# Optimization experiments

Hardware: AMD Instinct MI355X
Metric: run time of the kernel (lower is better)

Reference implementation:

```python
import jax, jax.numpy as jnp
import numpy as np

B, H, W = 32, 32, 32
C_CNN, C_EFF, HID = 512, 1280, 512


def conv1x1(x, w, b):
    # x: [B, Cin, H, W], w: [Cout, Cin], b: [Cout]
    return jnp.einsum('bchw,oc->bohw', x, w) + b[None, :, None, None]


def setup_inputs() -> dict:
    key = jax.random.key(0)
    ks = jax.random.split(key, 12)
    s = 0.02  # small init scale keeps softmax logits well-conditioned
    return {
        'cnn_features': jax.random.normal(ks[0], (B, C_CNN, H, W), jnp.float32),
        'efficient_features': jax.random.normal(ks[1], (B, C_EFF, H, W), jnp.float32),
        'W_cnn': jax.random.normal(ks[2], (HID, C_CNN), jnp.float32) * s,
        'b_cnn': jnp.zeros((HID,), jnp.float32),
        'W_eff': jax.random.normal(ks[3], (HID, C_EFF), jnp.float32) * s,
        'b_eff': jnp.zeros((HID,), jnp.float32),
        'W_q': jax.random.normal(ks[4], (HID, HID), jnp.float32) * s,
        'b_q': jnp.zeros((HID,), jnp.float32),
        'W_k': jax.random.normal(ks[5], (HID, HID), jnp.float32) * s,
        'b_k': jnp.zeros((HID,), jnp.float32),
        'W_v': jax.random.normal(ks[6], (HID, HID), jnp.float32) * s,
        'b_v': jnp.zeros((HID,), jnp.float32),
        'gamma': jnp.asarray([0.1], jnp.float32),
    }


def reference(cnn_features, efficient_features, W_cnn, b_cnn, W_eff, b_eff,
              W_q, b_q, W_k, b_k, W_v, b_v, gamma):
    cnn_proj = conv1x1(cnn_features, W_cnn, b_cnn)          # [B, HID, H, W]
    eff_proj = conv1x1(efficient_features, W_eff, b_eff)    # [B, HID, H, W]
    b, c, h, w = cnn_proj.shape
    n = h * w
    # 1x1 conv QKV projections then flatten spatial dims into tokens
    q = conv1x1(cnn_proj, W_q, b_q).reshape(b, c, n).transpose(0, 2, 1)  # [B, N, C]
    k = conv1x1(eff_proj, W_k, b_k).reshape(b, c, n)                     # [B, C, N]
    v = conv1x1(eff_proj, W_v, b_v).reshape(b, c, n).transpose(0, 2, 1)  # [B, N, C]
    attn = jax.nn.softmax(jnp.einsum('bnc,bcm->bnm', q, k), axis=-1)     # [B, N, N] (unscaled, as in source)
    out = jnp.einsum('bnm,bmc->bnc', attn, v)                            # [B, N, C]
    out = out.transpose(0, 2, 1).reshape(b, c, h, w)
    return gamma[0] * out + cnn_proj
```

## Files before the change

### kernel.cpp

```cpp
#include <hip/hip_runtime.h>
#include <hip/hip_bf16.h>
#include <cstdint>


typedef __hip_bfloat16 bf16;
typedef __bf16 bf16x8 __attribute__((ext_vector_type(8)));
typedef float f32x4 __attribute__((ext_vector_type(4)));

#define NB   32
#define NTOK 1024
#define NHID 512
#define CEFF 1280
#define WSZ  (NHID*NHID)

struct W4 { const float* s[4]; };
__global__ __launch_bounds__(256) void convert_w4_kernel(W4 w, bf16* __restrict__ dst) {
    int i = blockIdx.x * 256 + threadIdx.x;
    int sel = i >> 18, off = i & (WSZ - 1);
    dst[i] = __float2bfloat16(w.s[sel][off]);
}

__global__ __launch_bounds__(256) void transpose_to_bf16_kernel(const float* __restrict__ in,
                                                                bf16* __restrict__ out,
                                                                int C, int N) {
    __shared__ float tile[32][33];
    const int n0 = blockIdx.x * 32, c0 = blockIdx.y * 32, b = blockIdx.z;
    in  += (size_t)b * C * N;
    out += (size_t)b * N * C;
    const int tx = threadIdx.x, ty = threadIdx.y;
    #pragma unroll
    for (int i = ty; i < 32; i += 8)
        tile[i][tx] = in[(size_t)(c0 + i) * N + n0 + tx];
    __syncthreads();
    #pragma unroll
    for (int i = ty; i < 32; i += 8)
        out[(size_t)(n0 + i) * C + c0 + tx] = __float2bfloat16(tile[tx][i]);
}

__global__ __launch_bounds__(256) void bias_fuse_kernel(
    const float* __restrict__ Wq, const float* __restrict__ Wk, const float* __restrict__ Wv,
    const float* __restrict__ bc, const float* __restrict__ be,
    const float* __restrict__ bq, const float* __restrict__ bk, const float* __restrict__ bv,
    float* __restrict__ bqc, float* __restrict__ bkv) {
    const int r = blockIdx.x, t = threadIdx.x;
    const float* Wrow; const float* vin; float badd; float* dst;
    if (r < 512)       { Wrow = Wq + (size_t)r * 512;          vin = bc; badd = bq[r];        dst = bqc + r; }
    else if (r < 1024) { Wrow = Wk + (size_t)(r - 512) * 512;  vin = be; badd = bk[r - 512];  dst = bkv + (r - 512); }
    else               { Wrow = Wv + (size_t)(r - 1024) * 512; vin = be; badd = bv[r - 1024]; dst = bkv + (r - 512); }
    float s = Wrow[t] * vin[t] + Wrow[t + 256] * vin[t + 256];
    #pragma unroll
    for (int off = 32; off >= 1; off >>= 1) s += __shfl_xor(s, off, 64);
    __shared__ float red[4];
    if ((t & 63) == 0) red[t >> 6] = s;
    __syncthreads();
    if (t == 0) dst[0] = red[0] + red[1] + red[2] + red[3] + badd;
}

__global__ __launch_bounds__(256) void gemm_bt_kernel(
    const bf16* __restrict__ A, long long aStride, int lda,
    const bf16* __restrict__ Bt, long long bStride, int ldb,
    int K, int swiz,
    const float* __restrict__ bias,
    float* __restrict__ outF, long long fStride, int ldf,
    const bf16* __restrict__ residH, const float* __restrict__ gammaPtr,
    const float* __restrict__ rsumIn,
    float* __restrict__ rsumOut,
    bf16* __restrict__ outHt, long long htStride, int ldht, int htMax,
    bf16* __restrict__ outHn, long long hnStride, int ldhn, int hnBase, int doExp)
{
    __shared__ __bf16 lA[2][128 * 32];
    __shared__ __bf16 lB[2][128 * 32];
    __shared__ float lrs[128];

    const int tid  = threadIdx.x;
    const int wave = tid >> 6;
    const int lane = tid & 63;

    int bx, by, bz;
    if (swiz) { bx = (int)blockIdx.y & 7; by = (int)blockIdx.y >> 3; bz = (int)blockIdx.z * 8 + (int)blockIdx.x; }
    else      { bx = (int)blockIdx.x;     by = (int)blockIdx.y;      bz = (int)blockIdx.z; }
    const int m0 = by * 128;
    const int n0 = bx * 128;

    const bf16* Ab = A  + (size_t)bz * aStride;
    const bf16* Bb = Bt + (size_t)bz * bStride;

    const int wm = wave >> 1, wn = wave & 1;
    const int lrow = lane & 15, quad = lane >> 4;

    f32x4 acc[4][4];
    #pragma unroll
    for (int i = 0; i < 4; i++)
        #pragma unroll
        for (int j = 0; j < 4; j++)
            acc[i][j] = (f32x4){0.f, 0.f, 0.f, 0.f};

    const int rowl = lane >> 2;
    const int qsw  = (lane & 3) ^ ((lane >> 3) & 3);
    const bf16* gA0 = Ab + (size_t)(m0 +      wave * 16 + rowl) * lda + qsw * 8;
    const bf16* gA1 = Ab + (size_t)(m0 + 64 + wave * 16 + rowl) * lda + qsw * 8;
    const bf16* gB0 = Bb + (size_t)(n0 +      wave * 16 + rowl) * ldb + qsw * 8;
    const bf16* gB1 = Bb + (size_t)(n0 + 64 + wave * 16 + rowl) * ldb + qsw * 8;
    const int dst0 = (wave * 64) * 8;
    const int dst1 = (256 + wave * 64) * 8;

    const int sw = quad ^ ((lrow >> 1) & 3);
    int aoff[4], boff[4];
    #pragma unroll
    for (int mt = 0; mt < 4; mt++) aoff[mt] = ((wm * 4 + mt) * 64 + lrow * 4 + sw) * 8;
    #pragma unroll
    for (int nt = 0; nt < 4; nt++) boff[nt] = ((wn * 4 + nt) * 64 + lrow * 4 + sw) * 8;

    auto stage = [&](int k0, int b) {
        __builtin_amdgcn_global_load_lds((const __attribute__((address_space(1))) void*)(gA0 + k0),
                                         (__attribute__((address_space(3))) void*)(&lA[b][dst0]), 16, 0, 0);
        __builtin_amdgcn_global_load_lds((const __attribute__((address_space(1))) void*)(gA1 + k0),
                                         (__attribute__((address_space(3))) void*)(&lA[b][dst1]), 16, 0, 0);
        __builtin_amdgcn_global_load_lds((const __attribute__((address_space(1))) void*)(gB0 + k0),
                                         (__attribute__((address_space(3))) void*)(&lB[b][dst0]), 16, 0, 0);
        __builtin_amdgcn_global_load_lds((const __attribute__((address_space(1))) void*)(gB1 + k0),
                                         (__attribute__((address_space(3))) void*)(&lB[b][dst1]), 16, 0, 0);
    };

    auto compute = [&](int b) {
        const __bf16* __restrict__ pA = lA[b];
        const __bf16* __restrict__ pB = lB[b];
        bf16x8 af[4], bfr[4];
        #pragma unroll
        for (int mt = 0; mt < 4; mt++) af[mt]  = *(const bf16x8*)&pA[aoff[mt]];
        #pragma unroll
        for (int nt = 0; nt < 4; nt++) bfr[nt] = *(const bf16x8*)&pB[boff[nt]];
        #pragma unroll
        for (int mt = 0; mt < 4; mt++)
            #pragma unroll
            for (int nt = 0; nt < 4; nt++)
                acc[mt][nt] = __builtin_amdgcn_mfma_f32_16x16x32_bf16(af[mt], bfr[nt], acc[mt][nt], 0, 0, 0);
    };

    stage(0, 0);
    int cur = 0;
    for (int k0 = 32; k0 < K; k0 += 32) {
        stage(k0, cur ^ 1);
        asm volatile("s_waitcnt vmcnt(4)" ::: "memory");
        __builtin_amdgcn_s_barrier();
        asm volatile("" ::: "memory");
        compute(cur);
        asm volatile("s_waitcnt lgkmcnt(0)" ::: "memory");
        __builtin_amdgcn_s_barrier();
        cur ^= 1;
    }
    asm volatile("s_waitcnt vmcnt(0)" ::: "memory");
    __builtin_amdgcn_s_barrier();
    asm volatile("" ::: "memory");
    compute(cur);

    const float gscale = gammaPtr ? gammaPtr[0] : 1.0f;
    float rs[4][4];
    if (rsumOut)
        #pragma unroll
        for (int mt = 0; mt < 4; mt++)
            #pragma unroll
            for (int r = 0; r < 4; r++) rs[mt][r] = 0.f;

    #pragma unroll
    for (int mt = 0; mt < 4; mt++) {
        const int mbase = m0 + wm * 64 + mt * 16 + quad * 4;
        float bv[4];
        #pragma unroll
        for (int r = 0; r < 4; r++) bv[r] = bias ? bias[mbase + r] : 0.f;
        #pragma unroll
        for (int nt = 0; nt < 4; nt++) {
            const int n = n0 + wn * 64 + nt * 16 + lrow;
            float v[4];
            #pragma unroll
            for (int r = 0; r < 4; r++) {
                v[r] = acc[mt][nt][r] + bv[r];
                if (doExp) v[r] = __expf(v[r]);
                if (rsumOut) rs[mt][r] += v[r];
            }
            if (outF) {
                float* p = outF + (size_t)bz * fStride;
                const bf16* rp = residH + (size_t)bz * fStride;
                const float rinv = rsumIn ? 1.0f / rsumIn[(size_t)bz * NTOK + n] : 1.0f;
                #pragma unroll
                for (int r = 0; r < 4; r++) {
                    size_t idx = (size_t)(mbase + r) * ldf + n;
                    p[idx] = gscale * v[r] * rinv + __bfloat162float(rp[idx]);
                }
            }
            if (outHt && mbase < htMax) {
                union { bf16 h[4]; unsigned long long u; } pk;
                #pragma unroll
                for (int r = 0; r < 4; r++) pk.h[r] = __float2bfloat16(v[r]);
                *(unsigned long long*)&outHt[(size_t)bz * htStride + (size_t)n * ldht + mbase] = pk.u;
            }
            if (outHn && mbase >= hnBase) {
                bf16* p = outHn + (size_t)bz * hnStride;
                #pragma unroll
                for (int r = 0; r < 4; r++)
                    p[(size_t)(mbase - hnBase + r) * ldhn + n] = __float2bfloat16(v[r]);
            }
        }
    }

    if (rsumOut) {
        #pragma unroll
        for (int mt = 0; mt < 4; mt++)
            #pragma unroll
            for (int r = 0; r < 4; r++) {
                float s = rs[mt][r];
                s += __shfl_xor(s, 1, 64);
                s += __shfl_xor(s, 2, 64);
                s += __shfl_xor(s, 4, 64);
                s += __shfl_xor(s, 8, 64);
                rs[mt][r] = s;
            }
        if (tid < 128) lrs[tid] = 0.f;
        __syncthreads();
        if (lrow == 0) {
            #pragma unroll
            for (int mt = 0; mt < 4; mt++)
                #pragma unroll
                for (int r = 0; r < 4; r++)
                    atomicAdd(&lrs[wm * 64 + mt * 16 + quad * 4 + r], rs[mt][r]);
        }
        __syncthreads();
        if (tid < 128) atomicAdd(&rsumOut[(size_t)bz * NTOK + m0 + tid], lrs[tid]);
    }
}

extern "C" void kernel_launch(void* const* d_in, const int* in_sizes, int n_in,
                              void* d_out, int out_size, void* d_ws, size_t ws_size,
                              hipStream_t stream) {
    const float* x_cnn = (const float*)d_in[0];
    const float* x_eff = (const float*)d_in[1];
    const float* W_cnn = (const float*)d_in[2];
    const float* b_cnn = (const float*)d_in[3];
    const float* W_eff = (const float*)d_in[4];
    const float* b_eff = (const float*)d_in[5];
    const float* W_q   = (const float*)d_in[6];
    const float* b_q   = (const float*)d_in[7];
    const float* W_k   = (const float*)d_in[8];
    const float* b_k   = (const float*)d_in[9];
    const float* W_v   = (const float*)d_in[10];
    const float* b_v   = (const float*)d_in[11];
    const float* gamma = (const float*)d_in[12];
    float* out = (float*)d_out;

    uint8_t* ws = (uint8_t*)d_ws;
    size_t off = 0;
    auto alloc = [&](size_t bytes) -> uint8_t* {
        uint8_t* p = ws + off;
        off = (off + bytes + 255) & ~(size_t)255;
        return p;
    };

    bf16* Wall  = (bf16*)alloc((size_t)4 * WSZ * 2);
    bf16* Wc_h  = Wall;
    bf16* Wq_h  = Wall + WSZ;
    bf16* Wkv_h = Wall + 2 * (size_t)WSZ;
    bf16* Wct   = (bf16*)alloc((size_t)NHID * NHID * 2);
    bf16* Wet   = (bf16*)alloc((size_t)CEFF * NHID * 2);
    bf16* Wstack= (bf16*)alloc((size_t)1024 * NHID * 2);
    bf16* Wkve  = (bf16*)alloc((size_t)1024 * CEFF * 2);
    float* bstack = (float*)alloc(1024 * 4);
    float* bkv  = (float*)alloc(1024 * 4);
    float* rowSum = (float*)alloc((size_t)NB * NTOK * 4);
    bf16* Xc_t  = (bf16*)alloc((size_t)NB * NTOK * NHID * 2);
    bf16* Xe_t  = (bf16*)alloc((size_t)NB * NTOK * CEFF * 2);
    bf16* resid = (bf16*)alloc((size_t)NB * NHID * NTOK * 2);
    bf16* q_t   = (bf16*)alloc((size_t)NB * NTOK * NHID * 2);
    bf16* k_t   = (bf16*)alloc((size_t)NB * NTOK * NHID * 2);
    bf16* v_nt  = (bf16*)alloc((size_t)NB * NHID * NTOK * 2);
    bf16* P     = Xe_t;

    {
        W4 w; w.s[0] = W_cnn; w.s[1] = W_q; w.s[2] = W_k; w.s[3] = W_v;
        convert_w4_kernel<<<4 * WSZ / 256, 256, 0, stream>>>(w, Wall);
    }
    transpose_to_bf16_kernel<<<dim3(NHID / 32, NHID / 32, 1), dim3(32, 8), 0, stream>>>(W_cnn, Wct, NHID, NHID);
    transpose_to_bf16_kernel<<<dim3(CEFF / 32, NHID / 32, 1), dim3(32, 8), 0, stream>>>(W_eff, Wet, NHID, CEFF);

    transpose_to_bf16_kernel<<<dim3(NTOK / 32, NHID / 32, NB), dim3(32, 8), 0, stream>>>(x_cnn, Xc_t, NHID, NTOK);
    transpose_to_bf16_kernel<<<dim3(NTOK / 32, CEFF / 32, NB), dim3(32, 8), 0, stream>>>(x_eff, Xe_t, CEFF, NTOK);

    bias_fuse_kernel<<<1536, 256, 0, stream>>>(W_q, W_k, W_v, b_cnn, b_eff, b_q, b_k, b_v, bstack, bkv);
    hipMemcpyAsync(Wstack + (size_t)NHID * NHID, Wc_h, (size_t)NHID * NHID * 2,
                   hipMemcpyDeviceToDevice, stream);
    hipMemcpyAsync(bstack + NHID, b_cnn, NHID * 4, hipMemcpyDeviceToDevice, stream);

    hipMemsetAsync(rowSum, 0, (size_t)NB * NTOK * 4, stream);

    auto gemm = [&](dim3 grid, int swiz,
                    const bf16* A, long long aS, int lda,
                    const bf16* Bt, long long bS, int ldb, int K,
                    const float* bias,
                    float* oF, long long fS, int ldf, const bf16* rH, const float* gp,
                    const float* rIn, float* rOut,
                    bf16* oHt, long long htS, int ldht, int htMax,
                    bf16* oHn, long long hnS, int ldhn, int hnBase, int doExp) {
        gemm_bt_kernel<<<grid, 256, 0, stream>>>(A, aS, lda, Bt, bS, ldb, K, swiz, bias,
                                                 oF, fS, ldf, rH, gp, rIn, rOut,
                                                 oHt, htS, ldht, htMax, oHn, hnS, ldhn, hnBase, doExp);
    };

    const long long sNC = (long long)NTOK * NHID;
    const long long sCN = (long long)NHID * NTOK;
    const long long sNE = (long long)NTOK * CEFF;
    const long long sPP = (long long)NTOK * NTOK;

    gemm(dim3(4, 4, 1), 0, Wq_h, 0, NHID, Wct, 0, NHID, NHID, nullptr,
         nullptr, 0, 0, nullptr, nullptr, nullptr, nullptr,
         nullptr, 0, 0, 0, Wstack, 0, NHID, 0, 0);
    gemm(dim3(10, 8, 1), 0, Wkv_h, 0, NHID, Wet, 0, NHID, NHID, nullptr,
         nullptr, 0, 0, nullptr, nullptr, nullptr, nullptr,
         nullptr, 0, 0, 0, Wkve, 0, CEFF, 0, 0);

    gemm(dim3(8, 64, 4), 1, Wstack, 0, NHID, Xc_t, sNC, NHID, NHID, bstack,
         nullptr, 0, 0, nullptr, nullptr, nullptr, nullptr,
         q_t, sNC, NHID, NHID,
         resid, sCN, NTOK, NHID, 0);
    gemm(dim3(8, 64, 4), 1, Wkve, 0, CEFF, Xe_t, sNE, CEFF, CEFF, bkv,
         nullptr, 0, 0, nullptr, nullptr, nullptr, nullptr,
         k_t, sNC, NHID, NHID,
         v_nt, sCN, NTOK, NHID, 0);
    gemm(dim3(8, 64, 4), 1, q_t, sNC, NHID, k_t, sNC, NHID, NHID, nullptr,
         nullptr, 0, 0, nullptr, nullptr, nullptr, rowSum,
         nullptr, 0, 0, 0, P, sPP, NTOK, 0, 1);
    gemm(dim3(8, 32, 4), 1, v_nt, sCN, NTOK, P, sPP, NTOK, NTOK, nullptr,
         out, sCN, NTOK, resid, gamma, rowSum, nullptr,
         nullptr, 0, 0, 0, nullptr, 0, 0, 0, 0);
}
```

Baseline: 726.7 us.

## Enlarge GEMM tiles to 256x256 with 512-thread blocks

Doubles the GEMM block tile from 128x128 to 256x256 and uses 8 waves per block, each computing a 128x64 sub-tile with 8x4 MFMA accumulators. The grid swizzle becomes parameterised by a shift so the tile-index mapping fits the smaller grids. The larger tiles are meant to raise arithmetic intensity and cut global/LDS traffic per FLOP. In exchange, register pressure and LDS use per block double, which lowers occupancy and leaves fewer blocks in the small weight GEMMs and the batched launches.

```diff
diff --git a/kernel.cpp b/kernel.cpp
--- a/kernel.cpp
+++ b/kernel.cpp
@@ -56,10 +56,10 @@
     if (t == 0) dst[0] = red[0] + red[1] + red[2] + red[3] + badd;
 }
 
-__global__ __launch_bounds__(256) void gemm_bt_kernel(
+__global__ __launch_bounds__(512, 2) void gemm_bt_kernel(
     const bf16* __restrict__ A, long long aStride, int lda,
     const bf16* __restrict__ Bt, long long bStride, int ldb,
-    int K, int swiz,
+    int K, int swiz, int nxtShift,
     const float* __restrict__ bias,
     float* __restrict__ outF, long long fStride, int ldf,
     const bf16* __restrict__ residH, const float* __restrict__ gammaPtr,
@@ -68,48 +68,52 @@
     bf16* __restrict__ outHt, long long htStride, int ldht, int htMax,
     bf16* __restrict__ outHn, long long hnStride, int ldhn, int hnBase, int doExp)
 {
-    __shared__ __bf16 lA[2][128 * 32];
-    __shared__ __bf16 lB[2][128 * 32];
-    __shared__ float lrs[128];
+    __shared__ __bf16 lA[2][256 * 32];
+    __shared__ __bf16 lB[2][256 * 32];
+    __shared__ float lrs[256];
 
     const int tid  = threadIdx.x;
     const int wave = tid >> 6;
     const int lane = tid & 63;
 
     int bx, by, bz;
-    if (swiz) { bx = (int)blockIdx.y & 7; by = (int)blockIdx.y >> 3; bz = (int)blockIdx.z * 8 + (int)blockIdx.x; }
-    else      { bx = (int)blockIdx.x;     by = (int)blockIdx.y;      bz = (int)blockIdx.z; }
-    const int m0 = by * 128;
-    const int n0 = bx * 128;
+    if (swiz) {
+        int byR = (int)blockIdx.y;
+        bx = byR & ((1 << nxtShift) - 1);
+        by = byR >> nxtShift;
+        bz = (int)blockIdx.z * 8 + (int)blockIdx.x;
+    } else { bx = (int)blockIdx.x; by = (int)blockIdx.y; bz = (int)blockIdx.z; }
+    const int m0 = by * 256;
+    const int n0 = bx * 256;
 
     const bf16* Ab = A  + (size_t)bz * aStride;
     const bf16* Bb = Bt + (size_t)bz * bStride;
 
-    const int wm = wave >> 1, wn = wave & 1;
+    const int wm = wave >> 2, wn = wave & 3;
     const int lrow = lane & 15, quad = lane >> 4;
 
-    f32x4 acc[4][4];
-    #pragma unroll
-    for (int i = 0; i < 4; i++)
+    f32x4 acc[8][4];
+    #pragma unroll
+    for (int i = 0; i < 8; i++)
         #pragma unroll
         for (int j = 0; j < 4; j++)
             acc[i][j] = (f32x4){0.f, 0.f, 0.f, 0.f};
 
     const int rowl = lane >> 2;
     const int qsw  = (lane & 3) ^ ((lane >> 3) & 3);
-    const bf16* gA0 = Ab + (size_t)(m0 +      wave * 16 + rowl) * lda + qsw * 8;
-    const bf16* gA1 = Ab + (size_t)(m0 + 64 + wave * 16 + rowl) * lda + qsw * 8;
-    const bf16* gB0 = Bb + (size_t)(n0 +      wave * 16 + rowl) * ldb + qsw * 8;
-    const bf16* gB1 = Bb + (size_t)(n0 + 64 + wave * 16 + rowl) * ldb + qsw * 8;
+    const bf16* gA0 = Ab + (size_t)(m0 +       wave * 16 + rowl) * lda + qsw * 8;
+    const bf16* gA1 = Ab + (size_t)(m0 + 128 + wave * 16 + rowl) * lda + qsw * 8;
+    const bf16* gB0 = Bb + (size_t)(n0 +       wave * 16 + rowl) * ldb + qsw * 8;
+    const bf16* gB1 = Bb + (size_t)(n0 + 128 + wave * 16 + rowl) * ldb + qsw * 8;
     const int dst0 = (wave * 64) * 8;
-    const int dst1 = (256 + wave * 64) * 8;
+    const int dst1 = (512 + wave * 64) * 8;
 
     const int sw = quad ^ ((lrow >> 1) & 3);
-    int aoff[4], boff[4];
-    #pragma unroll
-    for (int mt = 0; mt < 4; mt++) aoff[mt] = ((wm * 4 + mt) * 64 + lrow * 4 + sw) * 8;
-    #pragma unroll
-    for (int nt = 0; nt < 4; nt++) boff[nt] = ((wn * 4 + nt) * 64 + lrow * 4 + sw) * 8;
+    int aoff[8], boff[4];
+    #pragma unroll
+    for (int mt = 0; mt < 8; mt++) aoff[mt] = ((wm * 128 + mt * 16 + lrow) * 4 + sw) * 8;
+    #pragma unroll
+    for (int nt = 0; nt < 4; nt++) boff[nt] = ((wn * 64 + nt * 16 + lrow) * 4 + sw) * 8;
 
     auto stage = [&](int k0, int b) {
         __builtin_amdgcn_global_load_lds((const __attribute__((address_space(1))) void*)(gA0 + k0),
@@ -125,13 +129,13 @@
     auto compute = [&](int b) {
         const __bf16* __restrict__ pA = lA[b];
         const __bf16* __restrict__ pB = lB[b];
-        bf16x8 af[4], bfr[4];
-        #pragma unroll
-        for (int mt = 0; mt < 4; mt++) af[mt]  = *(const bf16x8*)&pA[aoff[mt]];
+        bf16x8 af[8], bfr[4];
+        #pragma unroll
+        for (int mt = 0; mt < 8; mt++) af[mt]  = *(const bf16x8*)&pA[aoff[mt]];
         #pragma unroll
         for (int nt = 0; nt < 4; nt++) bfr[nt] = *(const bf16x8*)&pB[boff[nt]];
         #pragma unroll
-        for (int mt = 0; mt < 4; mt++)
+        for (int mt = 0; mt < 8; mt++)
             #pragma unroll
             for (int nt = 0; nt < 4; nt++)
                 acc[mt][nt] = __builtin_amdgcn_mfma_f32_16x16x32_bf16(af[mt], bfr[nt], acc[mt][nt], 0, 0, 0);
@@ -155,16 +159,16 @@
     compute(cur);
 
     const float gscale = gammaPtr ? gammaPtr[0] : 1.0f;
-    float rs[4][4];
+    float rs[8][4];
     if (rsumOut)
         #pragma unroll
-        for (int mt = 0; mt < 4; mt++)
+        for (int mt = 0; mt < 8; mt++)
             #pragma unroll
             for (int r = 0; r < 4; r++) rs[mt][r] = 0.f;
 
     #pragma unroll
-    for (int mt = 0; mt < 4; mt++) {
-        const int mbase = m0 + wm * 64 + mt * 16 + quad * 4;
+    for (int mt = 0; mt < 8; mt++) {
+        const int mbase = m0 + wm * 128 + mt * 16 + quad * 4;
         float bv[4];
         #pragma unroll
         for (int r = 0; r < 4; r++) bv[r] = bias ? bias[mbase + r] : 0.f;
@@ -205,7 +209,7 @@
 
     if (rsumOut) {
         #pragma unroll
-        for (int mt = 0; mt < 4; mt++)
+        for (int mt = 0; mt < 8; mt++)
             #pragma unroll
             for (int r = 0; r < 4; r++) {
                 float s = rs[mt][r];
@@ -215,17 +219,17 @@
                 s += __shfl_xor(s, 8, 64);
                 rs[mt][r] = s;
             }
-        if (tid < 128) lrs[tid] = 0.f;
+        if (tid < 256) lrs[tid] = 0.f;
         __syncthreads();
         if (lrow == 0) {
             #pragma unroll
-            for (int mt = 0; mt < 4; mt++)
+            for (int mt = 0; mt < 8; mt++)
                 #pragma unroll
                 for (int r = 0; r < 4; r++)
-                    atomicAdd(&lrs[wm * 64 + mt * 16 + quad * 4 + r], rs[mt][r]);
+                    atomicAdd(&lrs[wm * 128 + mt * 16 + quad * 4 + r], rs[mt][r]);
         }
         __syncthreads();
-        if (tid < 128) atomicAdd(&rsumOut[(size_t)bz * NTOK + m0 + tid], lrs[tid]);
+        if (tid < 256) atomicAdd(&rsumOut[(size_t)bz * NTOK + m0 + tid], lrs[tid]);
     }
 }
 
@@ -291,7 +295,7 @@
 
     hipMemsetAsync(rowSum, 0, (size_t)NB * NTOK * 4, stream);
 
-    auto gemm = [&](dim3 grid, int swiz,
+    auto gemm = [&](dim3 grid, int swiz, int nxtShift,
                     const bf16* A, long long aS, int lda,
                     const bf16* Bt, long long bS, int ldb, int K,
                     const float* bias,
@@ -299,7 +303,7 @@
                     const float* rIn, float* rOut,
                     bf16* oHt, long long htS, int ldht, int htMax,
                     bf16* oHn, long long hnS, int ldhn, int hnBase, int doExp) {
-        gemm_bt_kernel<<<grid, 256, 0, stream>>>(A, aS, lda, Bt, bS, ldb, K, swiz, bias,
+        gemm_bt_kernel<<<grid, 512, 0, stream>>>(A, aS, lda, Bt, bS, ldb, K, swiz, nxtShift, bias,
                                                  oF, fS, ldf, rH, gp, rIn, rOut,
                                                  oHt, htS, ldht, htMax, oHn, hnS, ldhn, hnBase, doExp);
     };
@@ -309,25 +313,25 @@
     const long long sNE = (long long)NTOK * CEFF;
     const long long sPP = (long long)NTOK * NTOK;
 
-    gemm(dim3(4, 4, 1), 0, Wq_h, 0, NHID, Wct, 0, NHID, NHID, nullptr,
+    gemm(dim3(2, 2, 1), 0, 0, Wq_h, 0, NHID, Wct, 0, NHID, NHID, nullptr,
          nullptr, 0, 0, nullptr, nullptr, nullptr, nullptr,
          nullptr, 0, 0, 0, Wstack, 0, NHID, 0, 0);
-    gemm(dim3(10, 8, 1), 0, Wkv_h, 0, NHID, Wet, 0, NHID, NHID, nullptr,
+    gemm(dim3(5, 4, 1), 0, 0, Wkv_h, 0, NHID, Wet, 0, NHID, NHID, nullptr,
          nullptr, 0, 0, nullptr, nullptr, nullptr, nullptr,
          nullptr, 0, 0, 0, Wkve, 0, CEFF, 0, 0);
 
-    gemm(dim3(8, 64, 4), 1, Wstack, 0, NHID, Xc_t, sNC, NHID, NHID, bstack,
+    gemm(dim3(8, 16, 4), 1, 2, Wstack, 0, NHID, Xc_t, sNC, NHID, NHID, bstack,
          nullptr, 0, 0, nullptr, nullptr, nullptr, nullptr,
          q_t, sNC, NHID, NHID,
          resid, sCN, NTOK, NHID, 0);
-    gemm(dim3(8, 64, 4), 1, Wkve, 0, CEFF, Xe_t, sNE, CEFF, CEFF, bkv,
+    gemm(dim3(8, 16, 4), 1, 2, Wkve, 0, CEFF, Xe_t, sNE, CEFF, CEFF, bkv,
          nullptr, 0, 0, nullptr, nullptr, nullptr, nullptr,
          k_t, sNC, NHID, NHID,
          v_nt, sCN, NTOK, NHID, 0);
-    gemm(dim3(8, 64, 4), 1, q_t, sNC, NHID, k_t, sNC, NHID, NHID, nullptr,
+    gemm(dim3(8, 16, 4), 1, 2, q_t, sNC, NHID, k_t, sNC, NHID, NHID, nullptr,
          nullptr, 0, 0, nullptr, nullptr, nullptr, rowSum,
          nullptr, 0, 0, 0, P, sPP, NTOK, 0, 1);
-    gemm(dim3(8, 32, 4), 1, v_nt, sCN, NTOK, P, sPP, NTOK, NTOK, nullptr,
+    gemm(dim3(8, 8, 4), 1, 2, v_nt, sCN, NTOK, P, sPP, NTOK, NTOK, nullptr,
          out, sCN, NTOK, resid, gamma, rowSum, nullptr,
          nullptr, 0, 0, 0, nullptr, 0, 0, 0, 0);
 }
```

Measured after the change: 738.9 us. Within noise of the previous version (+1.7%).
